# Optimization experiments

Hardware: AMD Instinct MI355X
Metric: run time of the kernel (lower is better)

Reference implementation:

```python
import jax, jax.numpy as jnp
import numpy as np

N = 256
MAX_LENGTH = 2048


def _hippo_legs_buffers(n, max_length):
    """Replicates HiPPO_LegS.__init__ precomputation (measure='legs', bilinear, dt=1)."""
    q = np.arange(n, dtype=np.float64)
    col, row = np.meshgrid(q, q)
    r = 2 * q + 1
    M = -(np.where(row >= col, r, 0) - np.diag(q))
    T = np.sqrt(2 * q + 1)
    A = (T[:, None] * M) / T[None, :]          # (N, N) LegS transition
    B = T.copy()                                # (N,) since B = sqrt(2n+1)
    evals = np.sqrt(2 * q + 1)

    t = np.arange(1, max_length + 1, dtype=np.float64)  # (L,)
    At = A[None, :, :] / t[:, None, None]                # (L, N, N)
    Bt = B[None, :] / t[:, None]                         # (L, N)
    I = np.eye(n)

    # bilinear discretization: (I - At/2) A_d = (I + At/2); (I - At/2) B_d = Bt
    lhs = I[None] - At / 2
    A_stacked = np.linalg.solve(lhs, I[None] + At / 2)               # (L, N, N)
    B_stacked = np.linalg.solve(lhs, Bt[..., None]).squeeze(-1)      # (L, N)

    C_stacked = (evals @ A)[None, :] / t[:, None]                    # (L, N)
    D_stacked = (evals @ B) / t                                      # (L,)
    scale = 1.0 / (1.0 - 0.5 * D_stacked)                            # dt = 1
    C_discr = scale[:, None] * 0.5 * C_stacked                       # (L, N)
    D_discr = (scale * (1.0 + 0.5 * D_stacked))[:, None]             # (L, 1)

    f32 = lambda x: jnp.asarray(x, dtype=jnp.float32)
    return f32(A_stacked), f32(B_stacked), f32(C_discr), f32(D_discr)


def setup_inputs() -> dict:
    key = jax.random.key(0)
    inputs = jax.random.normal(key, (MAX_LENGTH,), dtype=jnp.float32)
    A_stacked, B_stacked, C_discr_stacked, D_discr_stacked = _hippo_legs_buffers(N, MAX_LENGTH)
    return {
        "inputs": inputs,
        "A_stacked": A_stacked,
        "B_stacked": B_stacked,
        "C_discr_stacked": C_discr_stacked,
        "D_discr_stacked": D_discr_stacked,
    }


def reference(inputs, A_stacked, B_stacked, C_discr_stacked, D_discr_stacked):
    """inputs: (L,) -> next-step predictions (L, 1)."""
    L = inputs.shape[0]
    u = inputs[:, None]  # (L, 1)
    # first step uses dot(c, C), subsequent steps dot(2c, C)
    factor = jnp.where(jnp.arange(L) == 0, 1.0, 2.0).astype(inputs.dtype)

    def step(c, xs):
        A_i, B_i, C_i, D_i, u_i, f_i = xs
        c = A_i @ c + B_i * u_i              # (N,); F.linear(c, A) == A @ c
        pred = f_i * jnp.dot(c, C_i) + D_i * u_i  # (1,)
        return c, pred

    c0 = jnp.zeros((A_stacked.shape[-1],), dtype=inputs.dtype)
    _, preds = jax.lax.scan(
        step, c0,
        (A_stacked, B_stacked, C_discr_stacked, D_discr_stacked, u, factor),
    )
    return preds  # (L, 1)
```

## Files before the change

### kernel.cpp

```cpp
#include <hip/hip_runtime.h>

#define HIPPO_N 256
#define HIPPO_L 2048
#define CHUNKS  16
#define CSTEPS  128
#define NCOLS   257

#define WS_PHI    0
#define WS_Y0     (CHUNKS * HIPPO_N * HIPPO_N)
#define WS_R      (WS_Y0 + CHUNKS * HIPPO_N)
#define WS_PRED0  (WS_R + HIPPO_L * HIPPO_N)
#define WS_CIN    (WS_PRED0 + HIPPO_L)
#define WS_TOTAL  (WS_CIN + CHUNKS * HIPPO_N)


__global__ __launch_bounds__(256, 1)
void hippo_phase1(const float* __restrict__ u, float* __restrict__ ws) {
    const int lane = threadIdx.x & 63;
    const int wave = threadIdx.x >> 6;
    const int task = blockIdx.x * 4 + wave;
    if (task >= CHUNKS * NCOLS) return;
    const int g = task / NCOLS;
    const int j = task - g * NCOLS;
    const bool is_u = (j == HIPPO_N);
    const int i0 = lane * 4;

    float T[4], gv[4], fi1[4];
#pragma unroll
    for (int k = 0; k < 4; ++k) {
        const float fi = (float)(i0 + k);
        const float ip1 = fi + 1.0f;
        T[k] = sqrtf(2.0f * fi + 1.0f);
        fi1[k] = ip1;
        gv[k] = -T[k] * (ip1 + 65536.0f - ip1 * ip1);
    }

    float c[4];
#pragma unroll
    for (int k = 0; k < 4; ++k) c[k] = (!is_u && (i0 + k) == j) ? 1.0f : 0.0f;

    const int tbase = g * CSTEPS;
    float u_nxt = is_u ? u[tbase] : 0.0f;

    for (int tl = 0; tl < CSTEPS; ++tl) {
        const int t = tbase + tl + 1;
        const float u_t = u_nxt;
        if (is_u) {
            const int nxt = tbase + tl + 1;
            u_nxt = u[nxt < HIPPO_L ? nxt : HIPPO_L - 1];
        }
        const float two_t = 2.0f * (float)t;

        float pl[4];
        float run = 0.f;
#pragma unroll
        for (int k = 0; k < 4; ++k) { pl[k] = run; run += T[k] * c[k]; }
        float inc = run;
#pragma unroll
        for (int d = 1; d < 64; d <<= 1) {
            float w = __shfl_up(inc, d, 64);
            if (lane >= d) inc += w;
        }
        const float Pbase = inc - run;

        float vt[4], rho[4];
#pragma unroll
        for (int k = 0; k < 4; ++k) {
            const float P = Pbase + pl[k];
            vt[k] = c[k] * (two_t - fi1[k]) - T[k] * P + 2.0f * u_t * T[k];
            rho[k] = 1.0f / (two_t + fi1[k]);
        }

        float al[4], el[4];
        float Aacc = 1.f, Eacc = 0.f;
#pragma unroll
        for (int k = 0; k < 4; ++k) {
            al[k] = Aacc; el[k] = Eacc;
            const float a = (two_t - (fi1[k] - 1.0f)) * rho[k];
            const float e = T[k] * vt[k] * rho[k];
            Eacc = a * Eacc + e;
            Aacc = a * Aacc;
        }
        float Ai = Aacc, Ei = Eacc;
#pragma unroll
        for (int d = 1; d < 64; d <<= 1) {
            float Aw = __shfl_up(Ai, d, 64);
            float Ew = __shfl_up(Ei, d, 64);
            if (lane >= d) { Ei = Ai * Ew + Ei; Ai = Ai * Aw; }
        }
        float Qs = __shfl_up(Ei, 1, 64);
        if (lane == 0) Qs = 0.f;

        float s = 0.f;
#pragma unroll
        for (int k = 0; k < 4; ++k) {
            const float Q = al[k] * Qs + el[k];
            const float x = (vt[k] - T[k] * Q) * rho[k];
            c[k] = x;
            s += gv[k] * x;
        }
#pragma unroll
        for (int d = 32; d >= 1; d >>= 1) s += __shfl_xor(s, d, 64);

        if (lane == 0) {
            const float denom = two_t - 65536.0f;
            const float f = (t == 1) ? 1.0f : 2.0f;
            const float val = f * (s / denom);
            if (is_u)
                ws[WS_PRED0 + tbase + tl] = val + ((two_t + 65536.0f) / denom) * u_t;
            else
                ws[WS_R + (size_t)(tbase + tl) * HIPPO_N + j] = val;
        }
    }

    float4 cv; cv.x = c[0]; cv.y = c[1]; cv.z = c[2]; cv.w = c[3];
    if (is_u)
        *(float4*)(ws + WS_Y0 + g * HIPPO_N + i0) = cv;
    else
        *(float4*)(ws + WS_PHI + ((size_t)(g * HIPPO_N + j)) * HIPPO_N + i0) = cv;
}

__global__ __launch_bounds__(256, 1)
void hippo_phase2(float* __restrict__ ws) {
    __shared__ float cs[HIPPO_N];
    const int i = threadIdx.x;
    float c = 0.f;
    for (int g = 0; g < CHUNKS; ++g) {
        ws[WS_CIN + g * HIPPO_N + i] = c;
        cs[i] = c;
        __syncthreads();
        if (g < CHUNKS - 1) {
            const float* P = ws + WS_PHI + (size_t)g * HIPPO_N * HIPPO_N + i;
            float acc = ws[WS_Y0 + g * HIPPO_N + i];
#pragma unroll 8
            for (int jj = 0; jj < HIPPO_N; ++jj)
                acc += P[(size_t)jj * HIPPO_N] * cs[jj];
            c = acc;
        }
        __syncthreads();
    }
}

__global__ __launch_bounds__(256, 1)
void hippo_phase3(float* __restrict__ out, const float* __restrict__ ws) {
    const int lane = threadIdx.x & 63;
    const int wave = threadIdx.x >> 6;
    const int t = blockIdx.x * 4 + wave;
    if (t >= HIPPO_L) return;
    const int g = t / CSTEPS;
    const float* Rr = ws + WS_R + (size_t)t * HIPPO_N;
    const float* ci = ws + WS_CIN + g * HIPPO_N;
    const int i0 = lane * 4;
    const float4 r = *(const float4*)(Rr + i0);
    const float4 cv = *(const float4*)(ci + i0);
    float s = r.x * cv.x + r.y * cv.y + r.z * cv.z + r.w * cv.w;
#pragma unroll
    for (int d = 32; d >= 1; d >>= 1) s += __shfl_xor(s, d, 64);
    if (lane == 0) out[t] = ws[WS_PRED0 + t] + s;
}

__global__ __launch_bounds__(64, 1)
void hippo_scan_serial(const float* __restrict__ u, float* __restrict__ out) {
    const int lane = threadIdx.x & 63;
    const int i0 = lane * 4;
    float T[4], gv[4], fi1[4];
#pragma unroll
    for (int k = 0; k < 4; ++k) {
        const float fi = (float)(i0 + k);
        const float ip1 = fi + 1.0f;
        T[k] = sqrtf(2.0f * fi + 1.0f);
        fi1[k] = ip1;
        gv[k] = -T[k] * (ip1 + 65536.0f - ip1 * ip1);
    }
    float c[4] = {0.f, 0.f, 0.f, 0.f};
    float u_nxt = u[0];
    for (int t = 1; t <= HIPPO_L; ++t) {
        const float u_t = u_nxt;
        u_nxt = u[t < HIPPO_L ? t : HIPPO_L - 1];
        const float two_t = 2.0f * (float)t;
        float pl[4]; float run = 0.f;
#pragma unroll
        for (int k = 0; k < 4; ++k) { pl[k] = run; run += T[k] * c[k]; }
        float inc = run;
#pragma unroll
        for (int d = 1; d < 64; d <<= 1) {
            float w = __shfl_up(inc, d, 64);
            if (lane >= d) inc += w;
        }
        const float Pbase = inc - run;
        float vt[4], rho[4];
#pragma unroll
        for (int k = 0; k < 4; ++k) {
            const float P = Pbase + pl[k];
            vt[k] = c[k] * (two_t - fi1[k]) - T[k] * P + 2.0f * u_t * T[k];
            rho[k] = 1.0f / (two_t + fi1[k]);
        }
        float al[4], el[4]; float Aacc = 1.f, Eacc = 0.f;
#pragma unroll
        for (int k = 0; k < 4; ++k) {
            al[k] = Aacc; el[k] = Eacc;
            const float a = (two_t - (fi1[k] - 1.0f)) * rho[k];
            const float e = T[k] * vt[k] * rho[k];
            Eacc = a * Eacc + e; Aacc = a * Aacc;
        }
        float Ai = Aacc, Ei = Eacc;
#pragma unroll
        for (int d = 1; d < 64; d <<= 1) {
            float Aw = __shfl_up(Ai, d, 64);
            float Ew = __shfl_up(Ei, d, 64);
            if (lane >= d) { Ei = Ai * Ew + Ei; Ai = Ai * Aw; }
        }
        float Qs = __shfl_up(Ei, 1, 64);
        if (lane == 0) Qs = 0.f;
        float s = 0.f;
#pragma unroll
        for (int k = 0; k < 4; ++k) {
            const float Q = al[k] * Qs + el[k];
            const float x = (vt[k] - T[k] * Q) * rho[k];
            c[k] = x; s += gv[k] * x;
        }
#pragma unroll
        for (int d = 32; d >= 1; d >>= 1) s += __shfl_xor(s, d, 64);
        if (lane == 0) {
            const float denom = two_t - 65536.0f;
            const float f = (t == 1) ? 1.0f : 2.0f;
            out[t - 1] = f * (s / denom) + ((two_t + 65536.0f) / denom) * u_t;
        }
    }
}

extern "C" void kernel_launch(void* const* d_in, const int* in_sizes, int n_in,
                              void* d_out, int out_size, void* d_ws, size_t ws_size,
                              hipStream_t stream) {
    (void)in_sizes; (void)n_in; (void)out_size;
    const float* u = (const float*)d_in[0];
    float* out = (float*)d_out;

    if (ws_size < (size_t)WS_TOTAL * sizeof(float)) {
        hippo_scan_serial<<<dim3(1), dim3(64), 0, stream>>>(u, out);
        return;
    }
    float* ws = (float*)d_ws;
    const int p1_blocks = (CHUNKS * NCOLS + 3) / 4;
    hippo_phase1<<<dim3(p1_blocks), dim3(256), 0, stream>>>(u, ws);
    hippo_phase2<<<dim3(1), dim3(256), 0, stream>>>(ws);
    hippo_phase3<<<dim3(HIPPO_L / 4), dim3(256), 0, stream>>>(out, ws);
}
```

Measured before the change: 937.1 us.

## Fuse two wave scans into one affine scan and vectorize phase2 matvec

Phase1's per-step solve used two sequential wave-wide scans, a prefix sum followed by an affine recurrence. These are merged into a single combined 4-component scan, which removes one serial shuffle chain per timestep and uses the fast reciprocal builtin. Phase2's serial chunk-propagation matvec now splits the column range across four waves. Each thread loads float4 rows and sums partials through shared memory, cutting per-thread loop length. The fast reciprocal and the reordered arithmetic may change rounding slightly.

```diff
diff --git a/kernel.cpp b/kernel.cpp
--- a/kernel.cpp
+++ b/kernel.cpp
@@ -13,6 +13,20 @@
 #define WS_CIN    (WS_PRED0 + HIPPO_L)
 #define WS_TOTAL  (WS_CIN + CHUNKS * HIPPO_N)
 
+
+#define SCAN_STAGE(D)                                              \
+    {                                                              \
+        float Bw = __shfl_up(B, (D), 64);                          \
+        float Pw = __shfl_up(Pc, (D), 64);                         \
+        float Qw = __shfl_up(Qc, (D), 64);                         \
+        float Sw = __shfl_up(S, (D), 64);                          \
+        if (lane >= (D)) {                                         \
+            S  = Pc * Bw + Qc * Sw + S;                            \
+            Pc = Pc + Qc * Pw;                                     \
+            Qc = Qc * Qw;                                          \
+            B  = B + Bw;                                           \
+        }                                                          \
+    }
 
 __global__ __launch_bounds__(256, 1)
 void hippo_phase1(const float* __restrict__ u, float* __restrict__ ws) {
@@ -25,12 +39,14 @@
     const bool is_u = (j == HIPPO_N);
     const int i0 = lane * 4;
 
-    float T[4], gv[4], fi1[4];
+    float T[4], T2[4], fi[4], fi1[4], gv[4];
 #pragma unroll
     for (int k = 0; k < 4; ++k) {
-        const float fi = (float)(i0 + k);
-        const float ip1 = fi + 1.0f;
-        T[k] = sqrtf(2.0f * fi + 1.0f);
+        const float f = (float)(i0 + k);
+        const float ip1 = f + 1.0f;
+        T2[k] = 2.0f * f + 1.0f;
+        T[k] = sqrtf(T2[k]);
+        fi[k] = f;
         fi1[k] = ip1;
         gv[k] = -T[k] * (ip1 + 65536.0f - ip1 * ip1);
     }
@@ -50,62 +66,56 @@
             u_nxt = u[nxt < HIPPO_L ? nxt : HIPPO_L - 1];
         }
         const float two_t = 2.0f * (float)t;
-
-        float pl[4];
-        float run = 0.f;
-#pragma unroll
-        for (int k = 0; k < 4; ++k) { pl[k] = run; run += T[k] * c[k]; }
-        float inc = run;
-#pragma unroll
-        for (int d = 1; d < 64; d <<= 1) {
-            float w = __shfl_up(inc, d, 64);
-            if (lane >= d) inc += w;
-        }
-        const float Pbase = inc - run;
-
-        float vt[4], rho[4];
-#pragma unroll
-        for (int k = 0; k < 4; ++k) {
-            const float P = Pbase + pl[k];
-            vt[k] = c[k] * (two_t - fi1[k]) - T[k] * P + 2.0f * u_t * T[k];
-            rho[k] = 1.0f / (two_t + fi1[k]);
-        }
-
-        float al[4], el[4];
-        float Aacc = 1.f, Eacc = 0.f;
-#pragma unroll
-        for (int k = 0; k < 4; ++k) {
-            al[k] = Aacc; el[k] = Eacc;
-            const float a = (two_t - (fi1[k] - 1.0f)) * rho[k];
-            const float e = T[k] * vt[k] * rho[k];
-            Eacc = a * Eacc + e;
-            Aacc = a * Aacc;
-        }
-        float Ai = Aacc, Ei = Eacc;
-#pragma unroll
-        for (int d = 1; d < 64; d <<= 1) {
-            float Aw = __shfl_up(Ai, d, 64);
-            float Ew = __shfl_up(Ei, d, 64);
-            if (lane >= d) { Ei = Ai * Ew + Ei; Ai = Ai * Aw; }
-        }
-        float Qs = __shfl_up(Ei, 1, 64);
-        if (lane == 0) Qs = 0.f;
-
-        float s = 0.f;
-#pragma unroll
-        for (int k = 0; k < 4; ++k) {
-            const float Q = al[k] * Qs + el[k];
-            const float x = (vt[k] - T[k] * Q) * rho[k];
+        const float u2 = 2.0f * u_t;
+
+        float beta[4], pp[4], qq[4], ss[4], rho[4], alpha[4];
+#pragma unroll
+        for (int k = 0; k < 4; ++k) {
+            rho[k]   = __builtin_amdgcn_rcpf(two_t + fi1[k]);
+            beta[k]  = T[k] * c[k];
+            pp[k]    = -T2[k] * rho[k];
+            qq[k]    = (two_t - fi[k]) * rho[k];
+            alpha[k] = c[k] * (two_t - fi1[k]) + u2 * T[k];
+            ss[k]    = T[k] * rho[k] * alpha[k];
+        }
+
+        float B = beta[0], Pc = pp[0], Qc = qq[0], S = ss[0];
+#pragma unroll
+        for (int k = 1; k < 4; ++k) {
+            S  = pp[k] * B + qq[k] * S + ss[k];
+            Pc = pp[k] + qq[k] * Pc;
+            Qc = qq[k] * Qc;
+            B  = B + beta[k];
+        }
+
+        SCAN_STAGE(1)
+        SCAN_STAGE(2)
+        SCAN_STAGE(4)
+        SCAN_STAGE(8)
+        SCAN_STAGE(16)
+        SCAN_STAGE(32)
+
+        float Pin = __shfl_up(B, 1, 64);
+        float Qin = __shfl_up(S, 1, 64);
+        if (lane == 0) { Pin = 0.f; Qin = 0.f; }
+
+        float G = 0.f, P = Pin, Q = Qin;
+#pragma unroll
+        for (int k = 0; k < 4; ++k) {
+            const float x = rho[k] * (alpha[k] - T[k] * (P + Q));
+            G = fmaf(gv[k], x, G);
+            const float Qn = pp[k] * P + qq[k] * Q + ss[k];
+            P = P + beta[k];
+            Q = Qn;
             c[k] = x;
-            s += gv[k] * x;
-        }
-#pragma unroll
-        for (int d = 32; d >= 1; d >>= 1) s += __shfl_xor(s, d, 64);
+        }
+#pragma unroll
+        for (int d = 32; d >= 1; d >>= 1) G += __shfl_xor(G, d, 64);
 
         if (lane == 0) {
             const float denom = two_t - 65536.0f;
             const float f = (t == 1) ? 1.0f : 2.0f;
-            const float val = f * (s / denom);
+            const float val = f * (G / denom);
             if (is_u)
                 ws[WS_PRED0 + tbase + tl] = val + ((two_t + 65536.0f) / denom) * u_t;
             else
@@ -123,19 +133,35 @@
 __global__ __launch_bounds__(256, 1)
 void hippo_phase2(float* __restrict__ ws) {
     __shared__ float cs[HIPPO_N];
-    const int i = threadIdx.x;
+    __shared__ float partial[4][HIPPO_N];
+    const int tid = threadIdx.x;
+    const int wv = tid >> 6;
+    const int ln = tid & 63;
+    const int r0 = 4 * ln;
+
     float c = 0.f;
     for (int g = 0; g < CHUNKS; ++g) {
-        ws[WS_CIN + g * HIPPO_N + i] = c;
-        cs[i] = c;
+        ws[WS_CIN + g * HIPPO_N + tid] = c;
+        cs[tid] = c;
         __syncthreads();
         if (g < CHUNKS - 1) {
-            const float* P = ws + WS_PHI + (size_t)g * HIPPO_N * HIPPO_N + i;
-            float acc = ws[WS_Y0 + g * HIPPO_N + i];
-#pragma unroll 8
-            for (int jj = 0; jj < HIPPO_N; ++jj)
-                acc += P[(size_t)jj * HIPPO_N] * cs[jj];
-            c = acc;
+            const float* P = ws + WS_PHI + (size_t)g * HIPPO_N * HIPPO_N;
+            float a0 = 0.f, a1 = 0.f, a2 = 0.f, a3 = 0.f;
+#pragma unroll
+            for (int jj = 0; jj < 64; ++jj) {
+                const int j = 64 * wv + jj;
+                const float4 p = *(const float4*)(P + (size_t)j * HIPPO_N + r0);
+                const float csj = cs[j];
+                a0 = fmaf(p.x, csj, a0);
+                a1 = fmaf(p.y, csj, a1);
+                a2 = fmaf(p.z, csj, a2);
+                a3 = fmaf(p.w, csj, a3);
+            }
+            float4 pv; pv.x = a0; pv.y = a1; pv.z = a2; pv.w = a3;
+            *(float4*)&partial[wv][r0] = pv;
+            __syncthreads();
+            c = ws[WS_Y0 + g * HIPPO_N + tid] + partial[0][tid] + partial[1][tid]
+                + partial[2][tid] + partial[3][tid];
         }
         __syncthreads();
     }
```

Result: faster. 871.7 us (-7.0%).
